# Kernel tuning notes

Hardware: AMD Instinct MI355X
Metric: run time of the kernel (lower is better)

## Reference

```python
import jax, jax.numpy as jnp
import numpy as np


def _maxpool3d(x):
    # 3x3x3 max pool, stride 1, padding 1 (torch pads with -inf for max pool)
    return jax.lax.reduce_window(
        x, -jnp.inf, jax.lax.max,
        window_dimensions=(1, 1, 3, 3, 3),
        window_strides=(1, 1, 1, 1, 1),
        padding=[(0, 0), (0, 0), (1, 1), (1, 1), (1, 1)],
    )


def _soft_erode(x):
    return -_maxpool3d(-x)


def _soft_dilate(x):
    return _maxpool3d(x)


def _soft_open(x):
    return _soft_dilate(_soft_erode(x))


def setup_inputs() -> dict:
    key = jax.random.key(0)
    img = jax.random.uniform(key, (2, 1, 192, 256, 256), dtype=jnp.float32)
    return {"img": img}


def reference(img):
    # NOTE: in the original torch module, `skel` is computed via soft_close +
    # an iterative relu(skel - soft_open(skel)) loop, but the final line
    # `skel = F.relu(img - soft_open(img))` overwrites it entirely, so the
    # loop is dead code and the output depends only on img.
    opened = _soft_open(img)  # dilate(erode(img)), morphological opening
    return jax.nn.relu(img - opened)
```

## Files before the change

### kernel.cpp

```cpp
#include <hip/hip_runtime.h>
#include <math.h>


#define D_ 192
#define H_ 256
#define W_ 256
#define NB 2
#define TH 32
#define TW 64
#define CD 16
#define NCHUNK (D_ / CD)

#define RAW_H (TH + 4)
#define RAW_W (TW + 8)
#define RAW_S 76
#define EB_H  (TH + 2)
#define EB_W  (TW + 8)
#define EB_S  76

#define NRAWF4 (RAW_H * (RAW_W / 4))
#define NBTASK (EB_H * (EB_W / 8))

__device__ __forceinline__ float min3f(float a, float b, float c) {
    return fminf(fminf(a, b), c);
}
__device__ __forceinline__ float max3f(float a, float b, float c) {
    return fmaxf(fmaxf(a, b), c);
}

__global__ __launch_bounds__(256, 3)
void soft_skel_v2(const float* __restrict__ img, float* __restrict__ out) {
    __shared__ __align__(16) float raw[RAW_H][RAW_S];
    __shared__ __align__(16) float ebuf[EB_H][EB_S];

    const int tid = threadIdx.x;
    const int w0 = blockIdx.x * TW;
    const int h0 = blockIdx.y * TH;
    const int n  = blockIdx.z / NCHUNK;
    const int ch = blockIdx.z - n * NCHUNK;
    const int z0 = ch * CD;

    const float* vol  = img + (size_t)n * (D_ * H_ * W_);
    float*       ovol = out + (size_t)n * (D_ * H_ * W_);

    const float PINF = INFINITY;

    bool a_slot[3], a_img[3];
    int  a_lds[3], a_off[3];
    #pragma unroll
    for (int k = 0; k < 3; ++k) {
        int idx = tid + 256 * k;
        bool slot = idx < NRAWF4;
        int row = idx / (RAW_W / 4);
        int cg  = idx - row * (RAW_W / 4);
        int gh = h0 - 2 + row;
        int gw = w0 - 4 + 4 * cg;
        a_slot[k] = slot;
        a_img[k]  = slot && (gh >= 0) && (gh < H_) && (gw >= 0) && (gw <= W_ - 4);
        a_off[k]  = gh * W_ + gw;
        a_lds[k]  = slot ? (row * RAW_S + 4 * cg) : 0;
    }

    const int  r0 = tid / 9;
    const int  c0 = (tid - r0 * 9) * 8;
    const bool has1 = tid < (NBTASK - 256);
    const int  t1 = tid + 256;
    const int  r1 = t1 / 9;
    const int  c1 = (t1 - r1 * 9) * 8;

    const int ty = tid >> 3;
    const int xx = (tid & 7) * 8;

    float pm0[8], sp0[8], pm1[8], sp1[8];
    float t2A[8], t2B[8], t2C[8];
    float rwA[8], rwB[8], rwC[8];
    #pragma unroll
    for (int j = 0; j < 8; ++j) {
        pm0[j] = sp0[j] = pm1[j] = sp1[j] = PINF;
        t2A[j] = t2B[j] = 0.f;
        rwA[j] = rwB[j] = 0.f;
    }

    auto prefetch = [&](int zz, float4 L[3]) {
        const bool zok = (zz >= 0) && (zz < D_);
        const float* plane = vol + (size_t)zz * (H_ * W_);
        #pragma unroll
        for (int k = 0; k < 3; ++k) {
            float4 v = make_float4(PINF, PINF, PINF, PINF);
            if (zok && a_img[k]) v = *(const float4*)(plane + a_off[k]);
            L[k] = v;
        }
    };

    auto btask = [&](int r, int cb, float pm[8], float sp[8], bool zeok) {
        float vm[10];
        {
            const float* p0 = &raw[r][0];
            const float* p1 = &raw[r + 1][0];
            const float* p2 = &raw[r + 2][0];
            int cl = cb - 1; if (cl < 0) cl = 0;
            int cr = cb + 8; if (cr > RAW_W - 1) cr = RAW_W - 1;
            vm[0] = min3f(p0[cl], p1[cl], p2[cl]);
            vm[9] = min3f(p0[cr], p1[cr], p2[cr]);
            float4 q00 = *(const float4*)(p0 + cb);
            float4 q01 = *(const float4*)(p0 + cb + 4);
            float4 q10 = *(const float4*)(p1 + cb);
            float4 q11 = *(const float4*)(p1 + cb + 4);
            float4 q20 = *(const float4*)(p2 + cb);
            float4 q21 = *(const float4*)(p2 + cb + 4);
            vm[1] = min3f(q00.x, q10.x, q20.x);
            vm[2] = min3f(q00.y, q10.y, q20.y);
            vm[3] = min3f(q00.z, q10.z, q20.z);
            vm[4] = min3f(q00.w, q10.w, q20.w);
            vm[5] = min3f(q01.x, q11.x, q21.x);
            vm[6] = min3f(q01.y, q11.y, q21.y);
            vm[7] = min3f(q01.z, q11.z, q21.z);
            vm[8] = min3f(q01.w, q11.w, q21.w);
        }
        float s[8];
        #pragma unroll
        for (int j = 0; j < 8; ++j) s[j] = min3f(vm[j], vm[j + 1], vm[j + 2]);

        const bool rok = zeok && ((unsigned)(h0 - 1 + r) < (unsigned)H_);
        float e[8];
        #pragma unroll
        for (int j = 0; j < 8; ++j) {
            float ev = fminf(pm[j], s[j]);
            bool ok = rok && ((unsigned)(w0 - 4 + cb + j) < (unsigned)W_);
            e[j] = ok ? ev : -PINF;
            pm[j] = fminf(sp[j], s[j]);
            sp[j] = s[j];
        }
        *(float4*)&ebuf[r][cb]     = make_float4(e[0], e[1], e[2], e[3]);
        *(float4*)&ebuf[r][cb + 4] = make_float4(e[4], e[5], e[6], e[7]);
    };

    float4 L[3];
    prefetch(z0 - 2, L);
    const int zzend = z0 + CD + 1;

    for (int zz = z0 - 2; zz <= zzend; ++zz) {
        #pragma unroll
        for (int k = 0; k < 3; ++k)
            if (a_slot[k]) *(float4*)(&raw[0][0] + a_lds[k]) = L[k];
        if (zz < zzend) prefetch(zz + 1, L);
        __syncthreads();

        {
            float4 v0 = *(const float4*)&raw[ty + 2][xx + 4];
            float4 v1 = *(const float4*)&raw[ty + 2][xx + 8];
            rwC[0] = v0.x; rwC[1] = v0.y; rwC[2] = v0.z; rwC[3] = v0.w;
            rwC[4] = v1.x; rwC[5] = v1.y; rwC[6] = v1.z; rwC[7] = v1.w;
        }

        const int  ze   = zz - 1;
        const bool zeok = (ze >= 0) && (ze < D_);
        btask(r0, c0, pm0, sp0, zeok);
        if (has1) btask(r1, c1, pm1, sp1, zeok);
        __syncthreads();

        {
            float vm[10];
            const float* p0 = &ebuf[ty][0];
            const float* p1 = &ebuf[ty + 1][0];
            const float* p2 = &ebuf[ty + 2][0];
            vm[0] = max3f(p0[xx + 3], p1[xx + 3], p2[xx + 3]);
            vm[9] = max3f(p0[xx + 12], p1[xx + 12], p2[xx + 12]);
            float4 q00 = *(const float4*)(p0 + xx + 4);
            float4 q01 = *(const float4*)(p0 + xx + 8);
            float4 q10 = *(const float4*)(p1 + xx + 4);
            float4 q11 = *(const float4*)(p1 + xx + 8);
            float4 q20 = *(const float4*)(p2 + xx + 4);
            float4 q21 = *(const float4*)(p2 + xx + 8);
            vm[1] = max3f(q00.x, q10.x, q20.x);
            vm[2] = max3f(q00.y, q10.y, q20.y);
            vm[3] = max3f(q00.z, q10.z, q20.z);
            vm[4] = max3f(q00.w, q10.w, q20.w);
            vm[5] = max3f(q01.x, q11.x, q21.x);
            vm[6] = max3f(q01.y, q11.y, q21.y);
            vm[7] = max3f(q01.z, q11.z, q21.z);
            vm[8] = max3f(q01.w, q11.w, q21.w);
            #pragma unroll
            for (int j = 0; j < 8; ++j) t2C[j] = max3f(vm[j], vm[j + 1], vm[j + 2]);
        }

        if (zz >= z0 + 2) {
            const int z = zz - 2;
            float* op = ovol + ((size_t)z * H_ + (h0 + ty)) * W_ + (w0 + xx);
            float o[8];
            #pragma unroll
            for (int j = 0; j < 8; ++j) {
                float opened = max3f(t2A[j], t2B[j], t2C[j]);
                float v = rwA[j] - opened;
                o[j] = v > 0.f ? v : 0.f;
            }
            *(float4*)op       = make_float4(o[0], o[1], o[2], o[3]);
            *(float4*)(op + 4) = make_float4(o[4], o[5], o[6], o[7]);
        }

        #pragma unroll
        for (int j = 0; j < 8; ++j) {
            t2A[j] = t2B[j]; t2B[j] = t2C[j];
            rwA[j] = rwB[j]; rwB[j] = rwC[j];
        }
    }
}

extern "C" void kernel_launch(void* const* d_in, const int* in_sizes, int n_in,
                              void* d_out, int out_size, void* d_ws, size_t ws_size,
                              hipStream_t stream) {
    const float* img = (const float*)d_in[0];
    float* out = (float*)d_out;

    dim3 grid(W_ / TW, H_ / TH, NB * NCHUNK);
    dim3 block(256);
    soft_skel_v2<<<grid, block, 0, stream>>>(img, out);
}
```

Measured before the change: 194.8 us.

## Remap tile loads so each thread loads its own pixels plus halo, shrink depth chunk

Each thread now loads the two float4s of its own output pixels straight from global memory and keeps them in registers, instead of reading them back from LDS. A subset of 136 threads loads the halo ring. The erode task mapping is changed to row-major-by-column, the depth chunk drops from 16 to 12, and launch bounds rise to 4 blocks per SIMD. The smaller chunk adds more blocks and more z-halo overhead (16 planes per 12 outputs) in exchange for more occupancy and parallelism. The new task mapping may also change LDS bank behaviour.

```diff
diff --git a/kernel.cpp b/kernel.cpp
--- a/kernel.cpp
+++ b/kernel.cpp
@@ -8,18 +8,17 @@
 #define NB 2
 #define TH 32
 #define TW 64
-#define CD 16
+#define CD 12
 #define NCHUNK (D_ / CD)
 
 #define RAW_H (TH + 4)
 #define RAW_W (TW + 8)
 #define RAW_S 76
 #define EB_H  (TH + 2)
-#define EB_W  (TW + 8)
 #define EB_S  76
 
-#define NRAWF4 (RAW_H * (RAW_W / 4))
-#define NBTASK (EB_H * (EB_W / 8))
+#define NBTASK (EB_H * 9)
+#define NHALO  136
 
 __device__ __forceinline__ float min3f(float a, float b, float c) {
     return fminf(fminf(a, b), c);
@@ -28,8 +27,8 @@
     return fmaxf(fmaxf(a, b), c);
 }
 
-__global__ __launch_bounds__(256, 3)
-void soft_skel_v2(const float* __restrict__ img, float* __restrict__ out) {
+__global__ __launch_bounds__(256, 4)
+void soft_skel_v3(const float* __restrict__ img, float* __restrict__ out) {
     __shared__ __align__(16) float raw[RAW_H][RAW_S];
     __shared__ __align__(16) float ebuf[EB_H][EB_S];
 
@@ -45,31 +44,29 @@
 
     const float PINF = INFINITY;
 
-    bool a_slot[3], a_img[3];
-    int  a_lds[3], a_off[3];
-    #pragma unroll
-    for (int k = 0; k < 3; ++k) {
-        int idx = tid + 256 * k;
-        bool slot = idx < NRAWF4;
-        int row = idx / (RAW_W / 4);
-        int cg  = idx - row * (RAW_W / 4);
-        int gh = h0 - 2 + row;
-        int gw = w0 - 4 + 4 * cg;
-        a_slot[k] = slot;
-        a_img[k]  = slot && (gh >= 0) && (gh < H_) && (gw >= 0) && (gw <= W_ - 4);
-        a_off[k]  = gh * W_ + gw;
-        a_lds[k]  = slot ? (row * RAW_S + 4 * cg) : 0;
-    }
-
-    const int  r0 = tid / 9;
-    const int  c0 = (tid - r0 * 9) * 8;
+    const int ty = tid >> 3;
+    const int xx = (tid & 7) * 8;
+
+    const int own_goff = (h0 + ty) * W_ + (w0 + xx);
+    const int own_lds  = (ty + 2) * RAW_S + (xx + 4);
+
+    const bool h_has = tid < NHALO;
+    int h_r = 0, h_g = 0;
+    if (tid < 36)      { h_r = tid / 18;              h_g = tid % 18; }
+    else if (tid < 72) { h_r = 34 + (tid - 36) / 18;  h_g = (tid - 36) % 18; }
+    else               { int e = tid - 72; h_r = 2 + (e >> 1); h_g = (e & 1) ? 17 : 0; }
+    const int  h_gh  = h0 - 2 + h_r;
+    const int  h_gw  = w0 - 4 + 4 * h_g;
+    const bool h_img = h_has && (h_gh >= 0) && (h_gh < H_) && (h_gw >= 0) && (h_gw <= W_ - 4);
+    const int  h_goff = h_gh * W_ + h_gw;
+    const int  h_lds  = h_r * RAW_S + 4 * h_g;
+
+    const int  r0 = tid % EB_H;
+    const int  c0 = (tid / EB_H) * 8;
     const bool has1 = tid < (NBTASK - 256);
     const int  t1 = tid + 256;
-    const int  r1 = t1 / 9;
-    const int  c1 = (t1 - r1 * 9) * 8;
-
-    const int ty = tid >> 3;
-    const int xx = (tid & 7) * 8;
+    const int  r1 = t1 % EB_H;
+    const int  c1 = (t1 / EB_H) * 8;
 
     float pm0[8], sp0[8], pm1[8], sp1[8];
     float t2A[8], t2B[8], t2C[8];
@@ -84,11 +81,12 @@
     auto prefetch = [&](int zz, float4 L[3]) {
         const bool zok = (zz >= 0) && (zz < D_);
         const float* plane = vol + (size_t)zz * (H_ * W_);
-        #pragma unroll
-        for (int k = 0; k < 3; ++k) {
-            float4 v = make_float4(PINF, PINF, PINF, PINF);
-            if (zok && a_img[k]) v = *(const float4*)(plane + a_off[k]);
-            L[k] = v;
+        float4 pv = make_float4(PINF, PINF, PINF, PINF);
+        L[0] = pv; L[1] = pv; L[2] = pv;
+        if (zok) {
+            L[0] = *(const float4*)(plane + own_goff);
+            L[1] = *(const float4*)(plane + own_goff + 4);
+            if (h_img) L[2] = *(const float4*)(plane + h_goff);
         }
     };
 
@@ -140,18 +138,15 @@
     const int zzend = z0 + CD + 1;
 
     for (int zz = z0 - 2; zz <= zzend; ++zz) {
-        #pragma unroll
-        for (int k = 0; k < 3; ++k)
-            if (a_slot[k]) *(float4*)(&raw[0][0] + a_lds[k]) = L[k];
+        *(float4*)(&raw[0][0] + own_lds)     = L[0];
+        *(float4*)(&raw[0][0] + own_lds + 4) = L[1];
+        if (h_has) *(float4*)(&raw[0][0] + h_lds) = L[2];
+
+        rwC[0] = L[0].x; rwC[1] = L[0].y; rwC[2] = L[0].z; rwC[3] = L[0].w;
+        rwC[4] = L[1].x; rwC[5] = L[1].y; rwC[6] = L[1].z; rwC[7] = L[1].w;
+
         if (zz < zzend) prefetch(zz + 1, L);
         __syncthreads();
-
-        {
-            float4 v0 = *(const float4*)&raw[ty + 2][xx + 4];
-            float4 v1 = *(const float4*)&raw[ty + 2][xx + 8];
-            rwC[0] = v0.x; rwC[1] = v0.y; rwC[2] = v0.z; rwC[3] = v0.w;
-            rwC[4] = v1.x; rwC[5] = v1.y; rwC[6] = v1.z; rwC[7] = v1.w;
-        }
 
         const int  ze   = zz - 1;
         const bool zeok = (ze >= 0) && (ze < D_);
@@ -214,5 +209,5 @@
 
     dim3 grid(W_ / TW, H_ / TH, NB * NCHUNK);
     dim3 block(256);
-    soft_skel_v2<<<grid, block, 0, stream>>>(img, out);
-}
+    soft_skel_v3<<<grid, block, 0, stream>>>(img, out);
+}
```

After: 204.4 us. 1.05x slower.
